# Optimization experiments

Hardware: AMD Instinct MI355X
Metric: run time of the kernel (lower is better)

The kernel has to match this reference:

```python
import jax, jax.numpy as jnp
import numpy as np

N_NODES = 500_000
N_EDGES = 16_000_000
F_IN, F_HID, F_OUT = 5, 5, 8


def _gcn_conv(x, W, b, src, dst, norm, n):
    # x: [N, Fin] -> transform first (cheaper than transforming messages)
    h = x @ W                              # [N, Fout]
    msg = h[src] * norm[:, None]           # [E', Fout] gather + per-edge scale
    out = jax.ops.segment_sum(msg, dst, num_segments=n)  # scatter-add over dst
    return out + b


def setup_inputs() -> dict:
    key = jax.random.key(0)
    ks = jax.random.split(key, 6)
    x = jax.random.normal(ks[0], (N_NODES, F_IN), dtype=jnp.float32)
    edge_index = jax.random.randint(ks[1], (2, N_EDGES), 0, N_NODES, dtype=jnp.int32)
    # Glorot-ish init for the two GCNConv layers
    W1 = jax.random.normal(ks[2], (F_IN, F_HID), dtype=jnp.float32) / np.sqrt(F_IN)
    b1 = jnp.zeros((F_HID,), dtype=jnp.float32)
    W2 = jax.random.normal(ks[3], (F_HID, F_OUT), dtype=jnp.float32) / np.sqrt(F_HID)
    b2 = jnp.zeros((F_OUT,), dtype=jnp.float32)
    return {"x": x, "edge_index": edge_index, "W1": W1, "b1": b1, "W2": W2, "b2": b2}


def reference(x, edge_index, W1, b1, W2, b2):
    n = x.shape[0]
    # GCNConv default: add self-loops, symmetric D^-1/2 A D^-1/2 normalization
    loops = jnp.arange(n, dtype=edge_index.dtype)
    src = jnp.concatenate([edge_index[0], loops])
    dst = jnp.concatenate([edge_index[1], loops])
    deg = jax.ops.segment_sum(jnp.ones_like(dst, dtype=x.dtype), dst, num_segments=n)
    dinv = jnp.where(deg > 0, jax.lax.rsqrt(deg), 0.0)
    norm = dinv[src] * dinv[dst]           # [E + N]

    h = _gcn_conv(x, W1, b1, src, dst, norm, n)
    h = jax.nn.relu(h)
    # F.dropout with training=False is the identity (eval-mode reference)
    h = _gcn_conv(h, W2, b2, src, dst, norm, n)
    return jax.nn.log_softmax(h, axis=1)
```

## Files before the change

### kernel.cpp

```cpp
#include <hip/hip_runtime.h>
#include <math.h>


#define FIN 5
#define FHID 5
#define FOUT 8
#define RB 256
#define EPA 32768
#define NBUCK_MAX 2048
#define OCAP 10240

typedef _Float16 half8 __attribute__((ext_vector_type(8)));
typedef int int4v __attribute__((ext_vector_type(4)));
typedef float fl4 __attribute__((ext_vector_type(4)));


__global__ void k_scan1(const int* __restrict__ t, int* __restrict__ scn,
                        int* __restrict__ partial, int n) {
    __shared__ int sh[256];
    int tx = threadIdx.x;
    int i = blockIdx.x * 256 + tx;
    int v = (i < n) ? t[i] : 0;
    sh[tx] = v;
    __syncthreads();
    for (int off = 1; off < 256; off <<= 1) {
        int add = (tx >= off) ? sh[tx - off] : 0;
        __syncthreads();
        sh[tx] += add;
        __syncthreads();
    }
    if (i < n) scn[i] = sh[tx] - v;
    if (tx == 255) partial[blockIdx.x] = sh[255];
}

__global__ void k_scan2(int* __restrict__ partial, int nb) {
    __shared__ int sh[256];
    __shared__ int carry;
    int tx = threadIdx.x;
    if (tx == 0) carry = 0;
    __syncthreads();
    for (int base = 0; base < nb; base += 256) {
        int i = base + tx;
        int v = (i < nb) ? partial[i] : 0;
        int c0 = carry;
        sh[tx] = v;
        __syncthreads();
        for (int off = 1; off < 256; off <<= 1) {
            int add = (tx >= off) ? sh[tx - off] : 0;
            __syncthreads();
            sh[tx] += add;
            __syncthreads();
        }
        if (i < nb) partial[i] = c0 + sh[tx] - v;
        __syncthreads();
        if (tx == 0) carry = c0 + sh[255];
        __syncthreads();
    }
}


__global__ void k_histA(const int* __restrict__ dst, int* __restrict__ cnt,
                        int e, int nbuck, int nblkA) {
    __shared__ int hist[NBUCK_MAX];
    int tx = threadIdx.x, blk = blockIdx.x;
    for (int b = tx; b < nbuck; b += 1024) hist[b] = 0;
    __syncthreads();
    size_t base = (size_t)blk * EPA;
    const int4v* dst4 = (const int4v*)dst;
    for (int k = 0; k < EPA / 4096; ++k) {
        size_t e4 = base / 4 + (size_t)k * 1024 + tx;
        size_t i = e4 * 4;
        if (i + 3 < (size_t)e) {
            int4v d4 = __builtin_nontemporal_load(&dst4[e4]);
#pragma unroll
            for (int j = 0; j < 4; ++j) atomicAdd(&hist[d4[j] >> 8], 1);
        } else {
            for (int j = 0; j < 4; ++j) {
                size_t ii = i + j;
                if (ii < (size_t)e) atomicAdd(&hist[dst[ii] >> 8], 1);
            }
        }
    }
    __syncthreads();
    for (int b = tx; b < nbuck; b += 1024) cnt[(size_t)b * nblkA + blk] = hist[b];
}

__global__ void k_scatterA(const int* __restrict__ src, const int* __restrict__ dst,
                           const int* __restrict__ cnt,
                           const int* __restrict__ scn, const int* __restrict__ part,
                           unsigned int* __restrict__ binnedA,
                           int e, int nbuck, int nblkA) {
    __shared__ int lstart[NBUCK_MAX];
    __shared__ int cur[NBUCK_MAX];
    __shared__ int gbase[NBUCK_MAX];
    __shared__ unsigned int staged[EPA];
    int tx = threadIdx.x, blk = blockIdx.x;
    for (int b = tx; b < NBUCK_MAX; b += 1024) {
        if (b < nbuck) {
            size_t idx = (size_t)b * nblkA + blk;
            lstart[b] = cnt[idx];
            gbase[b] = scn[idx] + part[idx >> 8];
        } else {
            lstart[b] = 0;
        }
    }
    __syncthreads();
    int j0 = tx, j1 = tx + 1024;
    int c0 = lstart[j0], c1 = lstart[j1];
    for (int off = 1; off < NBUCK_MAX; off <<= 1) {
        int a0 = (j0 >= off) ? lstart[j0 - off] : 0;
        int a1 = (j1 >= off) ? lstart[j1 - off] : 0;
        __syncthreads();
        lstart[j0] += a0; lstart[j1] += a1;
        __syncthreads();
    }
    int e0 = lstart[j0] - c0, e1 = lstart[j1] - c1;
    __syncthreads();
    lstart[j0] = e0; lstart[j1] = e1;
    cur[j0] = e0;    cur[j1] = e1;
    __syncthreads();
    size_t base = (size_t)blk * EPA;
    const int4v* dst4 = (const int4v*)dst;
    const int4v* src4 = (const int4v*)src;
    for (int k = 0; k < EPA / 4096; ++k) {
        size_t e4 = base / 4 + (size_t)k * 1024 + tx;
        size_t i = e4 * 4;
        if (i + 3 < (size_t)e) {
            int4v d4 = __builtin_nontemporal_load(&dst4[e4]);
            int4v s4 = __builtin_nontemporal_load(&src4[e4]);
#pragma unroll
            for (int j = 0; j < 4; ++j) {
                int d = d4[j];
                int pos = atomicAdd(&cur[d >> 8], 1);
                staged[pos] = ((unsigned int)(d & (RB - 1)) << 19) | (unsigned int)s4[j];
            }
        } else {
            for (int j = 0; j < 4; ++j) {
                size_t ii = i + j;
                if (ii < (size_t)e) {
                    int d = dst[ii];
                    int pos = atomicAdd(&cur[d >> 8], 1);
                    staged[pos] = ((unsigned int)(d & (RB - 1)) << 19) | (unsigned int)src[ii];
                }
            }
        }
    }
    __syncthreads();
    int grp = tx >> 4, lane = tx & 15;
    for (int b = grp; b < nbuck; b += 64) {
        int ls = lstart[b];
        int le = (b + 1 < NBUCK_MAX) ? lstart[b + 1] : 0;
        int len = le - ls;
        int gb = gbase[b];
        for (int k = lane; k < len; k += 16)
            binnedA[gb + k] = staged[ls + k];
    }
}


__global__ void k_passC(const unsigned int* __restrict__ binnedA,
                        const int* __restrict__ scn, const int* __restrict__ part,
                        const float* __restrict__ x,
                        half8* __restrict__ g1, unsigned int* __restrict__ binned3,
                        int* __restrict__ nodeptr, int* __restrict__ midptr,
                        int n, int e, int nbuck, int nblkA, unsigned int half) {
    __shared__ int hist[2 * RB];
    __shared__ int scanbuf[2 * RB];
    __shared__ int cur[2 * RB];
    __shared__ unsigned int obuf[OCAP];
    int tx = threadIdx.x, b = blockIdx.x;
    hist[tx] = 0;
    __syncthreads();
    size_t i0 = (size_t)b * nblkA;
    int start = scn[i0] + part[i0 >> 8];
    int end;
    if (b + 1 < nbuck) {
        size_t i1 = (size_t)(b + 1) * nblkA;
        end = scn[i1] + part[i1 >> 8];
    } else {
        end = e;
    }
    int len = end - start;
    bool stage = (len <= OCAP);
    unsigned int r[20];
    if (stage) {
#pragma unroll
        for (int k = 0; k < 20; ++k) {
            int i = start + k * 512 + tx;
            if (i < end) {
                unsigned int p = binnedA[i];
                r[k] = p;
                int key = (int)((p >> 19) << 1) | ((p & 0x7FFFFu) >= half ? 1 : 0);
                atomicAdd(&hist[key], 1);
            }
        }
    } else {
        for (int i = start + tx; i < end; i += 512) {
            unsigned int p = binnedA[i];
            int key = (int)((p >> 19) << 1) | ((p & 0x7FFFFu) >= half ? 1 : 0);
            atomicAdd(&hist[key], 1);
        }
    }
    __syncthreads();
    int v = hist[tx];
    scanbuf[tx] = v;
    __syncthreads();
    for (int off = 1; off < 2 * RB; off <<= 1) {
        int add = (tx >= off) ? scanbuf[tx - off] : 0;
        __syncthreads();
        scanbuf[tx] += add;
        __syncthreads();
    }
    int excl = scanbuf[tx] - v;
    cur[tx] = excl;
    if ((tx & 1) == 0) nodeptr[(size_t)b * RB + (tx >> 1)] = start + excl;
    else               midptr[(size_t)b * RB + (tx >> 1)]  = start + excl;
    if (tx < RB) {
        int node = b * RB + tx;
        if (node < n) {
            int deg = hist[2 * tx] + hist[2 * tx + 1];
            float d = rsqrtf((float)(deg + 1));
            const float* xp = x + (size_t)node * FIN;
            half8 row = {};
#pragma unroll
            for (int f = 0; f < FIN; ++f) row[f] = (_Float16)(xp[f] * d);
            row[5] = (_Float16)d;
            g1[node] = row;
        }
    }
    if (b == nbuck - 1 && tx == 0) nodeptr[(size_t)nbuck * RB] = end;
    __syncthreads();
    if (stage) {
#pragma unroll
        for (int k = 0; k < 20; ++k) {
            int i = start + k * 512 + tx;
            if (i < end) {
                unsigned int p = r[k];
                int key = (int)((p >> 19) << 1) | ((p & 0x7FFFFu) >= half ? 1 : 0);
                int pos = atomicAdd(&cur[key], 1);
                obuf[pos] = p & 0x7FFFFu;
            }
        }
        __syncthreads();
        for (int j = tx; j < len; j += 512)
            binned3[start + j] = obuf[j];
    } else {
        for (int i = start + tx; i < end; i += 512) {
            unsigned int p = binnedA[i];
            int key = (int)((p >> 19) << 1) | ((p & 0x7FFFFu) >= half ? 1 : 0);
            int pos = atomicAdd(&cur[key], 1);
            binned3[start + pos] = p & 0x7FFFFu;
        }
    }
}


__global__ void k_vphase0(const unsigned int* __restrict__ ed,
                          const int* __restrict__ nodeptr, const int* __restrict__ midptr,
                          const half8* __restrict__ g,
                          fl4* __restrict__ acc4, float* __restrict__ acc1, int n) {
    int tid = blockIdx.x * blockDim.x + threadIdx.x;
    int node = tid >> 4;
    int lane = tid & 15;
    if (node >= n) return;
    int o0 = nodeptr[node];
    int om = midptr[node];
    float a0 = 0, a1 = 0, a2 = 0, a3 = 0, a4 = 0;
    for (int k = o0 + lane; k < om; k += 16) {
        unsigned int s = __builtin_nontemporal_load(&ed[k]);
        half8 hv = g[s];
        a0 += (float)hv[0]; a1 += (float)hv[1]; a2 += (float)hv[2];
        a3 += (float)hv[3]; a4 += (float)hv[4];
    }
#pragma unroll
    for (int off = 1; off < 16; off <<= 1) {
        a0 += __shfl_xor(a0, off, 16);
        a1 += __shfl_xor(a1, off, 16);
        a2 += __shfl_xor(a2, off, 16);
        a3 += __shfl_xor(a3, off, 16);
        a4 += __shfl_xor(a4, off, 16);
    }
    if (lane == 0) {
        fl4 p; p.x = a0; p.y = a1; p.z = a2; p.w = a3;
        __builtin_nontemporal_store(p, &acc4[node]);
        __builtin_nontemporal_store(a4, &acc1[node]);
    }
}

__global__ void k_vp1_l1(const unsigned int* __restrict__ ed,
                         const int* __restrict__ nodeptr, const int* __restrict__ midptr,
                         const half8* __restrict__ g1,
                         const fl4* __restrict__ acc4, const float* __restrict__ acc1,
                         const float* __restrict__ W1, const float* __restrict__ b1,
                         half8* __restrict__ g2, int n) {
    int tid = blockIdx.x * blockDim.x + threadIdx.x;
    int node = tid >> 4;
    int lane = tid & 15;
    if (node >= n) return;
    int om = midptr[node];
    int o1 = nodeptr[node + 1];
    float a0 = 0, a1 = 0, a2 = 0, a3 = 0, a4 = 0;
    for (int k = om + lane; k < o1; k += 16) {
        unsigned int s = __builtin_nontemporal_load(&ed[k]);
        half8 hv = g1[s];
        a0 += (float)hv[0]; a1 += (float)hv[1]; a2 += (float)hv[2];
        a3 += (float)hv[3]; a4 += (float)hv[4];
    }
#pragma unroll
    for (int off = 1; off < 16; off <<= 1) {
        a0 += __shfl_xor(a0, off, 16);
        a1 += __shfl_xor(a1, off, 16);
        a2 += __shfl_xor(a2, off, 16);
        a3 += __shfl_xor(a3, off, 16);
        a4 += __shfl_xor(a4, off, 16);
    }
    if (lane == 0) {
        fl4 pp = acc4[node];
        float p4 = acc1[node];
        half8 gi = g1[node];
        float d = (float)gi[5];
        float v[FIN];
        v[0] = (a0 + pp.x + (float)gi[0]) * d;
        v[1] = (a1 + pp.y + (float)gi[1]) * d;
        v[2] = (a2 + pp.z + (float)gi[2]) * d;
        v[3] = (a3 + pp.w + (float)gi[3]) * d;
        v[4] = (a4 + p4   + (float)gi[4]) * d;
        half8 go = {};
#pragma unroll
        for (int j = 0; j < FHID; ++j) {
            float s = b1[j];
#pragma unroll
            for (int k = 0; k < FIN; ++k) s = fmaf(v[k], W1[k * FHID + j], s);
            go[j] = (_Float16)(fmaxf(s, 0.0f) * d);
        }
        go[5] = gi[5];
        g2[node] = go;
    }
}

__global__ void k_vp1_l2(const unsigned int* __restrict__ ed,
                         const int* __restrict__ nodeptr, const int* __restrict__ midptr,
                         const half8* __restrict__ g2,
                         const fl4* __restrict__ acc4, const float* __restrict__ acc1,
                         const float* __restrict__ W2, const float* __restrict__ b2,
                         float* __restrict__ out, int n) {
    int tid = blockIdx.x * blockDim.x + threadIdx.x;
    int node = tid >> 4;
    int lane = tid & 15;
    if (node >= n) return;
    int om = midptr[node];
    int o1 = nodeptr[node + 1];
    float a0 = 0, a1 = 0, a2 = 0, a3 = 0, a4 = 0;
    for (int k = om + lane; k < o1; k += 16) {
        unsigned int s = __builtin_nontemporal_load(&ed[k]);
        half8 hv = g2[s];
        a0 += (float)hv[0]; a1 += (float)hv[1]; a2 += (float)hv[2];
        a3 += (float)hv[3]; a4 += (float)hv[4];
    }
#pragma unroll
    for (int off = 1; off < 16; off <<= 1) {
        a0 += __shfl_xor(a0, off, 16);
        a1 += __shfl_xor(a1, off, 16);
        a2 += __shfl_xor(a2, off, 16);
        a3 += __shfl_xor(a3, off, 16);
        a4 += __shfl_xor(a4, off, 16);
    }
    fl4 pp = acc4[node];
    float p4 = acc1[node];
    half8 gi = g2[node];
    float d = (float)gi[5];
    float v[FHID];
    v[0] = (a0 + pp.x + (float)gi[0]) * d;
    v[1] = (a1 + pp.y + (float)gi[1]) * d;
    v[2] = (a2 + pp.z + (float)gi[2]) * d;
    v[3] = (a3 + pp.w + (float)gi[3]) * d;
    v[4] = (a4 + p4   + (float)gi[4]) * d;
    int j = lane & 7;
    float oj = b2[j];
#pragma unroll
    for (int k = 0; k < FHID; ++k) oj = fmaf(v[k], W2[k * FOUT + j], oj);
    float mx = oj;
#pragma unroll
    for (int off = 1; off < 8; off <<= 1) mx = fmaxf(mx, __shfl_xor(mx, off, 8));
    float ex = expf(oj - mx);
    float ss = ex;
#pragma unroll
    for (int off = 1; off < 8; off <<= 1) ss += __shfl_xor(ss, off, 8);
    if (lane < 8) out[(size_t)node * FOUT + j] = oj - mx - logf(ss);
}


__global__ void f_init_deg(float* __restrict__ deg, int n) {
    int i = blockIdx.x * blockDim.x + threadIdx.x;
    if (i < n) deg[i] = 1.0f;
}
__global__ void f_count_deg(const int* __restrict__ dst, float* __restrict__ deg, int e) {
    int i = blockIdx.x * blockDim.x + threadIdx.x;
    if (i < e) atomicAdd(&deg[dst[i]], 1.0f);
}
__global__ void f_finish_deg_g1(const float* __restrict__ x, float* __restrict__ dinv,
                                float* __restrict__ g1, int n) {
    int i = blockIdx.x * blockDim.x + threadIdx.x;
    if (i >= n) return;
    float d = rsqrtf(dinv[i]);
    dinv[i] = d;
#pragma unroll
    for (int f = 0; f < FIN; ++f) g1[(size_t)i * FIN + f] = x[(size_t)i * FIN + f] * d;
}
__global__ void f_scatter5(const int* __restrict__ src, const int* __restrict__ dst,
                           const float* __restrict__ g, float* __restrict__ acc, int e) {
    int i = blockIdx.x * blockDim.x + threadIdx.x;
    if (i >= e) return;
    int s = src[i], d = dst[i];
    float* a = acc + (size_t)d * 5;
    const float* gp = g + (size_t)s * 5;
    atomicAdd(a + 0, gp[0]);
    atomicAdd(a + 1, gp[1]);
    atomicAdd(a + 2, gp[2]);
    atomicAdd(a + 3, gp[3]);
    atomicAdd(a + 4, gp[4]);
}
__global__ void f_update1(const float* __restrict__ dinv, float* __restrict__ g,
                          float* __restrict__ acc, const float* __restrict__ W1,
                          const float* __restrict__ b1, int n) {
    int i = blockIdx.x * blockDim.x + threadIdx.x;
    if (i >= n) return;
    float d = dinv[i];
    float v[FIN];
#pragma unroll
    for (int f = 0; f < FIN; ++f) {
        size_t idx = (size_t)i * FIN + f;
        v[f] = (acc[idx] + g[idx]) * d;
        acc[idx] = 0.0f;
    }
#pragma unroll
    for (int j = 0; j < FHID; ++j) {
        float s = b1[j];
#pragma unroll
        for (int k = 0; k < FIN; ++k) s += v[k] * W1[k * FHID + j];
        g[(size_t)i * FHID + j] = fmaxf(s, 0.0f) * d;
    }
}
__global__ void f_update2(const float* __restrict__ dinv, const float* __restrict__ g,
                          const float* __restrict__ acc, const float* __restrict__ W2,
                          const float* __restrict__ b2, float* __restrict__ out, int n) {
    int i = blockIdx.x * blockDim.x + threadIdx.x;
    if (i >= n) return;
    float d = dinv[i];
    float v[FHID];
#pragma unroll
    for (int f = 0; f < FHID; ++f) v[f] = (acc[(size_t)i * FHID + f] + g[(size_t)i * FHID + f]) * d;
    float o[FOUT];
    float m = -1e30f;
#pragma unroll
    for (int j = 0; j < FOUT; ++j) {
        float s = b2[j];
#pragma unroll
        for (int k = 0; k < FHID; ++k) s += v[k] * W2[k * FOUT + j];
        o[j] = s;
        m = fmaxf(m, s);
    }
    float ssum = 0.0f;
#pragma unroll
    for (int j = 0; j < FOUT; ++j) ssum += expf(o[j] - m);
    float lse = m + logf(ssum);
#pragma unroll
    for (int j = 0; j < FOUT; ++j) out[(size_t)i * FOUT + j] = o[j] - lse;
}


extern "C" void kernel_launch(void* const* d_in, const int* in_sizes, int n_in,
                              void* d_out, int out_size, void* d_ws, size_t ws_size,
                              hipStream_t stream) {
    const float* x  = (const float*)d_in[0];
    const int*   ei = (const int*)d_in[1];
    const float* W1 = (const float*)d_in[2];
    const float* b1 = (const float*)d_in[3];
    const float* W2 = (const float*)d_in[4];
    const float* b2 = (const float*)d_in[5];

    const int n = in_sizes[0] / FIN;
    const int e = in_sizes[1] / 2;
    const int* src = ei;
    const int* dst = ei + e;

    const int nbuck = (n + RB - 1) / RB;
    const int nblkA = (e + EPA - 1) / EPA;
    const size_t m = (size_t)nbuck * nblkA;
    const int nsb = (int)((m + 255) / 256);

    size_t off = 0;
    auto al = [&](size_t bytes) { size_t o = off; off = (off + bytes + 15) & ~(size_t)15; return o; };
    int*          cnt     = (int*)((char*)d_ws + al(m * 4));
    int*          scn     = (int*)((char*)d_ws + al(m * 4));
    int*          part    = (int*)((char*)d_ws + al((size_t)nsb * 4));
    int*          nptr    = (int*)((char*)d_ws + al(((size_t)nbuck * RB + 1) * 4));
    int*          mptr    = (int*)((char*)d_ws + al((size_t)nbuck * RB * 4));
    half8*        g1      = (half8*)((char*)d_ws + al((size_t)n * 16));
    unsigned int* binnedA = (unsigned int*)((char*)d_ws + al((size_t)e * 4));
    unsigned int* binned3 = (unsigned int*)((char*)d_ws + al((size_t)e * 4));
    half8*        g2      = (half8*)binnedA;
    fl4*          acc4    = (fl4*)((char*)binnedA + (size_t)16 * 1024 * 1024);
    float*        acc1    = (float*)((char*)binnedA + (size_t)32 * 1024 * 1024);
    const size_t need = off;

    if (ws_size >= need && n <= 524288 && n >= 1 && (e & 3) == 0 && nbuck <= NBUCK_MAX &&
        (size_t)e * 4 >= (size_t)34 * 1024 * 1024 && (size_t)n * 16 <= (size_t)16 * 1024 * 1024) {
        const unsigned int half = (unsigned int)(n >> 1);
        k_histA<<<nblkA, 1024, 0, stream>>>(dst, cnt, e, nbuck, nblkA);
        k_scan1<<<nsb, 256, 0, stream>>>(cnt, scn, part, (int)m);
        k_scan2<<<1, 256, 0, stream>>>(part, nsb);
        k_scatterA<<<nblkA, 1024, 0, stream>>>(src, dst, cnt, scn, part, binnedA, e, nbuck, nblkA);
        k_passC<<<nbuck, 512, 0, stream>>>(binnedA, scn, part, x, g1, binned3, nptr, mptr,
                                           n, e, nbuck, nblkA, half);
        const int ga = (int)(((size_t)n * 16 + 511) / 512);
        k_vphase0<<<ga, 512, 0, stream>>>(binned3, nptr, mptr, g1, acc4, acc1, n);
        k_vp1_l1<<<ga, 512, 0, stream>>>(binned3, nptr, mptr, g1, acc4, acc1, W1, b1, g2, n);
        k_vphase0<<<ga, 512, 0, stream>>>(binned3, nptr, mptr, g2, acc4, acc1, n);
        k_vp1_l2<<<ga, 512, 0, stream>>>(binned3, nptr, mptr, g2, acc4, acc1, W2, b2, (float*)d_out, n);
        return;
    }

    const int B = 256;
    const int gn = (n + B - 1) / B;
    const int ge = (e + B - 1) / B;
    float* fdinv = (float*)d_ws;
    float* fg    = fdinv + n;
    float* facc  = fg + (size_t)5 * n;
    hipMemsetAsync(facc, 0, (size_t)5 * n * sizeof(float), stream);
    f_init_deg<<<gn, B, 0, stream>>>(fdinv, n);
    f_count_deg<<<ge, B, 0, stream>>>(dst, fdinv, e);
    f_finish_deg_g1<<<gn, B, 0, stream>>>(x, fdinv, fg, n);
    f_scatter5<<<ge, B, 0, stream>>>(src, dst, fg, facc, e);
    f_update1<<<gn, B, 0, stream>>>(fdinv, fg, facc, W1, b1, n);
    f_scatter5<<<ge, B, 0, stream>>>(src, dst, fg, facc, e);
    f_update2<<<gn, B, 0, stream>>>(fdinv, fg, facc, W2, b2, (float*)d_out, n);
}
```

Baseline: 451.9 us.

## Group edges by source half per bucket instead of interleaving halves per node

Changes the per-bucket sort key so that, inside each 256-node bucket, all edges with sources in the low half come first, then all edges with sources in the high half, rather than interleaving the two halves for each node. Each gather phase now reads one contiguous region of the edge array per bucket, which is meant to improve streaming locality of the edge index reads and to keep gathered source rows within one half of the feature table. End offsets are derived from the next node's pointer, with a special case at the last node of a bucket. The cost is slightly more index arithmetic and a branch when loading offsets.

```diff
diff --git a/kernel.cpp b/kernel.cpp
--- a/kernel.cpp
+++ b/kernel.cpp
@@ -162,7 +162,7 @@
                         const int* __restrict__ scn, const int* __restrict__ part,
                         const float* __restrict__ x,
                         half8* __restrict__ g1, unsigned int* __restrict__ binned3,
-                        int* __restrict__ nodeptr, int* __restrict__ midptr,
+                        int* __restrict__ p0ptr, int* __restrict__ p1ptr,
                         int n, int e, int nbuck, int nblkA, unsigned int half) {
     __shared__ int hist[2 * RB];
     __shared__ int scanbuf[2 * RB];
@@ -190,14 +190,14 @@
             if (i < end) {
                 unsigned int p = binnedA[i];
                 r[k] = p;
-                int key = (int)((p >> 19) << 1) | ((p & 0x7FFFFu) >= half ? 1 : 0);
+                int key = ((p & 0x7FFFFu) >= half ? 256 : 0) | (int)(p >> 19);
                 atomicAdd(&hist[key], 1);
             }
         }
     } else {
         for (int i = start + tx; i < end; i += 512) {
             unsigned int p = binnedA[i];
-            int key = (int)((p >> 19) << 1) | ((p & 0x7FFFFu) >= half ? 1 : 0);
+            int key = ((p & 0x7FFFFu) >= half ? 256 : 0) | (int)(p >> 19);
             atomicAdd(&hist[key], 1);
         }
     }
@@ -213,12 +213,12 @@
     }
     int excl = scanbuf[tx] - v;
     cur[tx] = excl;
-    if ((tx & 1) == 0) nodeptr[(size_t)b * RB + (tx >> 1)] = start + excl;
-    else               midptr[(size_t)b * RB + (tx >> 1)]  = start + excl;
+    if (tx < 256) p0ptr[(size_t)b * RB + tx] = start + excl;
+    else          p1ptr[(size_t)b * RB + (tx - 256)] = start + excl;
     if (tx < RB) {
         int node = b * RB + tx;
         if (node < n) {
-            int deg = hist[2 * tx] + hist[2 * tx + 1];
+            int deg = hist[tx] + hist[256 + tx];
             float d = rsqrtf((float)(deg + 1));
             const float* xp = x + (size_t)node * FIN;
             half8 row = {};
@@ -228,7 +228,7 @@
             g1[node] = row;
         }
     }
-    if (b == nbuck - 1 && tx == 0) nodeptr[(size_t)nbuck * RB] = end;
+    if (b == nbuck - 1 && tx == 0) p0ptr[(size_t)nbuck * RB] = end;
     __syncthreads();
     if (stage) {
 #pragma unroll
@@ -236,7 +236,7 @@
             int i = start + k * 512 + tx;
             if (i < end) {
                 unsigned int p = r[k];
-                int key = (int)((p >> 19) << 1) | ((p & 0x7FFFFu) >= half ? 1 : 0);
+                int key = ((p & 0x7FFFFu) >= half ? 256 : 0) | (int)(p >> 19);
                 int pos = atomicAdd(&cur[key], 1);
                 obuf[pos] = p & 0x7FFFFu;
             }
@@ -247,7 +247,7 @@
     } else {
         for (int i = start + tx; i < end; i += 512) {
             unsigned int p = binnedA[i];
-            int key = (int)((p >> 19) << 1) | ((p & 0x7FFFFu) >= half ? 1 : 0);
+            int key = ((p & 0x7FFFFu) >= half ? 256 : 0) | (int)(p >> 19);
             int pos = atomicAdd(&cur[key], 1);
             binned3[start + pos] = p & 0x7FFFFu;
         }
@@ -256,17 +256,18 @@
 
 
 __global__ void k_vphase0(const unsigned int* __restrict__ ed,
-                          const int* __restrict__ nodeptr, const int* __restrict__ midptr,
+                          const int* __restrict__ p0, const int* __restrict__ p1,
                           const half8* __restrict__ g,
                           fl4* __restrict__ acc4, float* __restrict__ acc1, int n) {
     int tid = blockIdx.x * blockDim.x + threadIdx.x;
     int node = tid >> 4;
     int lane = tid & 15;
     if (node >= n) return;
-    int o0 = nodeptr[node];
-    int om = midptr[node];
+    int dl = node & (RB - 1);
+    int o0 = p0[node];
+    int oe = (dl == RB - 1) ? p1[node & ~(RB - 1)] : p0[node + 1];
     float a0 = 0, a1 = 0, a2 = 0, a3 = 0, a4 = 0;
-    for (int k = o0 + lane; k < om; k += 16) {
+    for (int k = o0 + lane; k < oe; k += 16) {
         unsigned int s = __builtin_nontemporal_load(&ed[k]);
         half8 hv = g[s];
         a0 += (float)hv[0]; a1 += (float)hv[1]; a2 += (float)hv[2];
@@ -288,7 +289,7 @@
 }
 
 __global__ void k_vp1_l1(const unsigned int* __restrict__ ed,
-                         const int* __restrict__ nodeptr, const int* __restrict__ midptr,
+                         const int* __restrict__ p0, const int* __restrict__ p1,
                          const half8* __restrict__ g1,
                          const fl4* __restrict__ acc4, const float* __restrict__ acc1,
                          const float* __restrict__ W1, const float* __restrict__ b1,
@@ -297,10 +298,11 @@
     int node = tid >> 4;
     int lane = tid & 15;
     if (node >= n) return;
-    int om = midptr[node];
-    int o1 = nodeptr[node + 1];
+    int dl = node & (RB - 1);
+    int o0 = p1[node];
+    int oe = (dl == RB - 1) ? p0[(node & ~(RB - 1)) + RB] : p1[node + 1];
     float a0 = 0, a1 = 0, a2 = 0, a3 = 0, a4 = 0;
-    for (int k = om + lane; k < o1; k += 16) {
+    for (int k = o0 + lane; k < oe; k += 16) {
         unsigned int s = __builtin_nontemporal_load(&ed[k]);
         half8 hv = g1[s];
         a0 += (float)hv[0]; a1 += (float)hv[1]; a2 += (float)hv[2];
@@ -339,7 +341,7 @@
 }
 
 __global__ void k_vp1_l2(const unsigned int* __restrict__ ed,
-                         const int* __restrict__ nodeptr, const int* __restrict__ midptr,
+                         const int* __restrict__ p0, const int* __restrict__ p1,
                          const half8* __restrict__ g2,
                          const fl4* __restrict__ acc4, const float* __restrict__ acc1,
                          const float* __restrict__ W2, const float* __restrict__ b2,
@@ -348,10 +350,11 @@
     int node = tid >> 4;
     int lane = tid & 15;
     if (node >= n) return;
-    int om = midptr[node];
-    int o1 = nodeptr[node + 1];
+    int dl = node & (RB - 1);
+    int o0 = p1[node];
+    int oe = (dl == RB - 1) ? p0[(node & ~(RB - 1)) + RB] : p1[node + 1];
     float a0 = 0, a1 = 0, a2 = 0, a3 = 0, a4 = 0;
-    for (int k = om + lane; k < o1; k += 16) {
+    for (int k = o0 + lane; k < oe; k += 16) {
         unsigned int s = __builtin_nontemporal_load(&ed[k]);
         half8 hv = g2[s];
         a0 += (float)hv[0]; a1 += (float)hv[1]; a2 += (float)hv[2];
@@ -494,8 +497,8 @@
     int*          cnt     = (int*)((char*)d_ws + al(m * 4));
     int*          scn     = (int*)((char*)d_ws + al(m * 4));
     int*          part    = (int*)((char*)d_ws + al((size_t)nsb * 4));
-    int*          nptr    = (int*)((char*)d_ws + al(((size_t)nbuck * RB + 1) * 4));
-    int*          mptr    = (int*)((char*)d_ws + al((size_t)nbuck * RB * 4));
+    int*          p0ptr   = (int*)((char*)d_ws + al(((size_t)nbuck * RB + 1) * 4));
+    int*          p1ptr   = (int*)((char*)d_ws + al((size_t)nbuck * RB * 4));
     half8*        g1      = (half8*)((char*)d_ws + al((size_t)n * 16));
     unsigned int* binnedA = (unsigned int*)((char*)d_ws + al((size_t)e * 4));
     unsigned int* binned3 = (unsigned int*)((char*)d_ws + al((size_t)e * 4));
@@ -511,13 +514,13 @@
         k_scan1<<<nsb, 256, 0, stream>>>(cnt, scn, part, (int)m);
         k_scan2<<<1, 256, 0, stream>>>(part, nsb);
         k_scatterA<<<nblkA, 1024, 0, stream>>>(src, dst, cnt, scn, part, binnedA, e, nbuck, nblkA);
-        k_passC<<<nbuck, 512, 0, stream>>>(binnedA, scn, part, x, g1, binned3, nptr, mptr,
+        k_passC<<<nbuck, 512, 0, stream>>>(binnedA, scn, part, x, g1, binned3, p0ptr, p1ptr,
                                            n, e, nbuck, nblkA, half);
         const int ga = (int)(((size_t)n * 16 + 511) / 512);
-        k_vphase0<<<ga, 512, 0, stream>>>(binned3, nptr, mptr, g1, acc4, acc1, n);
-        k_vp1_l1<<<ga, 512, 0, stream>>>(binned3, nptr, mptr, g1, acc4, acc1, W1, b1, g2, n);
-        k_vphase0<<<ga, 512, 0, stream>>>(binned3, nptr, mptr, g2, acc4, acc1, n);
-        k_vp1_l2<<<ga, 512, 0, stream>>>(binned3, nptr, mptr, g2, acc4, acc1, W2, b2, (float*)d_out, n);
+        k_vphase0<<<ga, 512, 0, stream>>>(binned3, p0ptr, p1ptr, g1, acc4, acc1, n);
+        k_vp1_l1<<<ga, 512, 0, stream>>>(binned3, p0ptr, p1ptr, g1, acc4, acc1, W1, b1, g2, n);
+        k_vphase0<<<ga, 512, 0, stream>>>(binned3, p0ptr, p1ptr, g2, acc4, acc1, n);
+        k_vp1_l2<<<ga, 512, 0, stream>>>(binned3, p0ptr, p1ptr, g2, acc4, acc1, W2, b2, (float*)d_out, n);
         return;
     }
 
```

New measurement: 452.1 us. Within noise of the previous version (+0.1%).
